# Optimization experiments

Measured on AMD Instinct MI355X. Metric: run time of the kernel, lower is better.

Reference implementation:

```python
import jax, jax.numpy as jnp
import numpy as np


def setup_inputs() -> dict:
    key = jax.random.key(0)
    ks = jax.random.split(key, 4)
    B, T, D, H = 64, 512, 512, 1024
    return {
        "x": jax.random.normal(ks[0], (B, T, D), dtype=jnp.float32),
        "kz": jax.random.normal(ks[1], (D, H), dtype=jnp.float32) * (1.0 / np.sqrt(D)),
        "kr": jax.random.normal(ks[2], (D, H), dtype=jnp.float32) * (1.0 / np.sqrt(D)),
        "kh": jax.random.normal(ks[3], (D, H), dtype=jnp.float32) * (1.0 / np.sqrt(D)),
        "mz": jnp.ones((H,), dtype=jnp.float32),
        "mr": jnp.ones((H,), dtype=jnp.float32),
        "br": jnp.zeros((H,), dtype=jnp.float32),
        "bz": jnp.zeros((H,), dtype=jnp.float32),
    }


def reference(x, kz, kr, kh, mz, mr, br, bz):
    B, T, D = x.shape
    H = kz.shape[1]
    # Precompute input projections for all timesteps (batched GEMMs),
    # identical math to per-step matmuls in the original cell.
    xz = jnp.einsum("btd,dh->bth", x, kz)  # [B,T,H]
    xr = jnp.einsum("btd,dh->bth", x, kr)
    xh = jnp.einsum("btd,dh->bth", x, kh)

    def step(h, inp):
        xz_t, xr_t, xh_t = inp  # each [B,H]
        r = jnp.tanh(xr_t + h * mr + br) + 1.0
        z = jax.nn.sigmoid(xz_t + h * mz + bz)
        h_new = z * h + (1.0 - z) * jnp.tanh(xh_t + r * h)
        return h_new, h_new

    h0 = jnp.zeros((B, H), dtype=x.dtype)
    # scan over time axis: move T to leading dim
    xs = (jnp.swapaxes(xz, 0, 1), jnp.swapaxes(xr, 0, 1), jnp.swapaxes(xh, 0, 1))
    _, ys = jax.lax.scan(step, h0, xs)  # ys: [T,B,H]
    return jnp.swapaxes(ys, 0, 1)  # [B,T,H]
```

## Files before the change

kernel.cpp:

```cpp
#include <hip/hip_runtime.h>
#include <hip/hip_bf16.h>
#include <math.h>


#define M_DIM 32768
#define K_DIM 512
#define H_DIM 1024
#define HPAD  1088
#define N3    3072

typedef _Float16 half8v __attribute__((ext_vector_type(8)));
typedef _Float16 half4v __attribute__((ext_vector_type(4)));
typedef float f32x4 __attribute__((ext_vector_type(4)));

__device__ __forceinline__ f32x4 mfma16(half8v a, half8v b, f32x4 c) {
    return __builtin_amdgcn_mfma_f32_16x16x32_f16(a, b, c, 0, 0, 0);
}

__device__ __forceinline__ void load_lds16(const void* g, void* l) {
    __builtin_amdgcn_global_load_lds(
        (const __attribute__((address_space(1))) void*)g,
        (__attribute__((address_space(3))) void*)l, 16, 0, 0);
}

__global__ __launch_bounds__(256) void convert_x(
    const float4* __restrict__ x4, half4v* __restrict__ hi4,
    half4v* __restrict__ lo4, int n4)
{
    int i = blockIdx.x * 256 + threadIdx.x;
    if (i >= n4) return;
    float4 v = x4[i];
    half4v h, lo;
    h.x = (_Float16)v.x; lo.x = (_Float16)(v.x - (float)h.x);
    h.y = (_Float16)v.y; lo.y = (_Float16)(v.y - (float)h.y);
    h.z = (_Float16)v.z; lo.z = (_Float16)(v.z - (float)h.z);
    h.w = (_Float16)v.w; lo.w = (_Float16)(v.w - (float)h.w);
    hi4[i] = h; lo4[i] = lo;
}

__global__ __launch_bounds__(256) void convert_wt_t(
    const float* __restrict__ kz, const float* __restrict__ kr,
    const float* __restrict__ kh, _Float16* __restrict__ wth,
    _Float16* __restrict__ wtl)
{
    __shared__ float lds[64][65];
    const int bid = blockIdx.x;
    const int w = bid >> 7;
    const int rem = bid & 127;
    const int k0 = (rem >> 4) * 64;
    const int n0 = (rem & 15) * 64;
    const int tid = threadIdx.x;
    const float* s = (w == 0) ? kz : ((w == 1) ? kr : kh);

#pragma unroll
    for (int r = 0; r < 4; ++r) {
        const int kk = (tid >> 4) + r * 16;
        const int nn = (tid & 15) * 4;
        float4 v = *(const float4*)&s[(size_t)(k0 + kk) * H_DIM + n0 + nn];
        lds[kk][nn + 0] = v.x; lds[kk][nn + 1] = v.y;
        lds[kk][nn + 2] = v.z; lds[kk][nn + 3] = v.w;
    }
    __syncthreads();
#pragma unroll
    for (int r = 0; r < 4; ++r) {
        const int nr = (tid >> 4) + r * 16;
        const int kb = (tid & 15) * 4;
        half4v hi, lo;
#pragma unroll
        for (int i = 0; i < 4; ++i) {
            float v = lds[kb + i][nr];
            _Float16 h = (_Float16)v;
            hi[i] = h; lo[i] = (_Float16)(v - (float)h);
        }
        const size_t o = ((size_t)(w * H_DIM + n0 + nr)) * K_DIM + k0 + kb;
        *(half4v*)&wth[o] = hi;
        *(half4v*)&wtl[o] = lo;
    }
}

template<bool PAD>
__global__ __launch_bounds__(256) void gemm_mfma_split(
    const _Float16* __restrict__ Ahi, const _Float16* __restrict__ Alo,
    const _Float16* __restrict__ Bthi, const _Float16* __restrict__ Btlo,
    float* __restrict__ XZ, float* __restrict__ XR, float* __restrict__ OUT)
{
    __shared__ _Float16 Ah[128 * 32];
    __shared__ _Float16 Al[128 * 32];
    __shared__ _Float16 Bh[128 * 32];
    __shared__ _Float16 Bl[128 * 32];

    const int tid = threadIdx.x;
    const int w = tid >> 6, l = tid & 63;
    const int l15 = l & 15, quad = l >> 4;
    const int bx = blockIdx.x, by = blockIdx.y;
    const long m0 = (long)by * 128;
    const long n0 = (long)bx * 128;

    f32x4 acc[4][4] = {};

    const int s1 = tid, s2 = tid + 256;
    const long aoff1 = (m0 + (s1 >> 2)) * K_DIM + (s1 & 3) * 8;
    const long aoff2 = (m0 + (s2 >> 2)) * K_DIM + (s2 & 3) * 8;
    const long boff1 = (n0 + (s1 >> 2)) * K_DIM + (s1 & 3) * 8;
    const long boff2 = (n0 + (s2 >> 2)) * K_DIM + (s2 & 3) * 8;

    const _Float16* a1 = Ahi + aoff1;  const _Float16* a2 = Ahi + aoff2;
    const _Float16* q1 = Alo + aoff1;  const _Float16* q2 = Alo + aoff2;
    const _Float16* b1 = Bthi + boff1; const _Float16* b2 = Bthi + boff2;
    const _Float16* c1 = Btlo + boff1; const _Float16* c2 = Btlo + boff2;

    _Float16* ldsA1 = &Ah[w * 512]; _Float16* ldsA2 = &Ah[2048 + w * 512];
    _Float16* ldsQ1 = &Al[w * 512]; _Float16* ldsQ2 = &Al[2048 + w * 512];
    _Float16* ldsB1 = &Bh[w * 512]; _Float16* ldsB2 = &Bh[2048 + w * 512];
    _Float16* ldsC1 = &Bl[w * 512]; _Float16* ldsC2 = &Bl[2048 + w * 512];

    const int wm = (w >> 1) * 64, wn = (w & 1) * 64;

    for (int kk = 0; kk < K_DIM / 32; ++kk) {
        load_lds16(a1, ldsA1); load_lds16(a2, ldsA2);
        load_lds16(q1, ldsQ1); load_lds16(q2, ldsQ2);
        load_lds16(b1, ldsB1); load_lds16(b2, ldsB2);
        load_lds16(c1, ldsC1); load_lds16(c2, ldsC2);
        a1 += 32; a2 += 32; q1 += 32; q2 += 32;
        b1 += 32; b2 += 32; c1 += 32; c2 += 32;
        __syncthreads();

        half8v afh[4], afl[4], bfh[4], bfl[4];
#pragma unroll
        for (int mi = 0; mi < 4; ++mi) {
            int row = (wm + mi * 16 + l15) * 32 + quad * 8;
            afh[mi] = *(const half8v*)&Ah[row];
            afl[mi] = *(const half8v*)&Al[row];
        }
#pragma unroll
        for (int ni = 0; ni < 4; ++ni) {
            int row = (wn + ni * 16 + l15) * 32 + quad * 8;
            bfh[ni] = *(const half8v*)&Bh[row];
            bfl[ni] = *(const half8v*)&Bl[row];
        }
#pragma unroll
        for (int mi = 0; mi < 4; ++mi)
#pragma unroll
            for (int ni = 0; ni < 4; ++ni) {
                acc[mi][ni] = mfma16(afh[mi], bfh[ni], acc[mi][ni]);
                acc[mi][ni] = mfma16(afh[mi], bfl[ni], acc[mi][ni]);
                acc[mi][ni] = mfma16(afl[mi], bfh[ni], acc[mi][ni]);
            }
        __syncthreads();
    }

    const long stride = PAD ? HPAD : H_DIM;
    float* dst = (bx < 8) ? XZ : ((bx < 16) ? XR : OUT);
    const long nl = (long)(bx & 7) * 128 + wn + l15;
#pragma unroll
    for (int mi = 0; mi < 4; ++mi) {
        const long m = m0 + wm + mi * 16 + quad * 4;
#pragma unroll
        for (int ni = 0; ni < 4; ++ni) {
            float* p = dst + m * stride + nl + ni * 16;
#pragma unroll
            for (int i = 0; i < 4; ++i)
                p[(long)i * stride] = acc[mi][ni][i];
        }
    }
}

#define BM 128
#define BN 128
#define BK 8
__global__ __launch_bounds__(256) void gemm_f32(
    const float* __restrict__ A, const float* __restrict__ B,
    float* __restrict__ C, int M, int N, int K)
{
    __shared__ float As[BK][BM];
    __shared__ float Bs[BK][BN];
    const int tid = threadIdx.x;
    const int bm = blockIdx.y * BM, bn = blockIdx.x * BN;
    const int tx = tid & 15, ty = tid >> 4;
    float acc[8][8];
#pragma unroll
    for (int i = 0; i < 8; i++)
#pragma unroll
        for (int j = 0; j < 8; j++) acc[i][j] = 0.f;
    const int a_row = tid >> 1, a_k = (tid & 1) * 4;
    const int b_row = tid >> 5, b_col = (tid & 31) * 4;
    const float* Aptr = A + (size_t)(bm + a_row) * K + a_k;
    const float* Bptr = B + (size_t)b_row * N + bn + b_col;
    for (int k0 = 0; k0 < K; k0 += BK) {
        float4 av = *(const float4*)(Aptr + k0);
        float4 bv = *(const float4*)(Bptr + (size_t)k0 * N);
        As[a_k + 0][a_row] = av.x; As[a_k + 1][a_row] = av.y;
        As[a_k + 2][a_row] = av.z; As[a_k + 3][a_row] = av.w;
        *(float4*)&Bs[b_row][b_col] = bv;
        __syncthreads();
#pragma unroll
        for (int kk = 0; kk < BK; kk++) {
            float4 a0 = *(const float4*)&As[kk][ty * 8];
            float4 a1 = *(const float4*)&As[kk][ty * 8 + 4];
            float4 b0 = *(const float4*)&Bs[kk][tx * 8];
            float4 b1 = *(const float4*)&Bs[kk][tx * 8 + 4];
            float a[8] = {a0.x, a0.y, a0.z, a0.w, a1.x, a1.y, a1.z, a1.w};
            float b[8] = {b0.x, b0.y, b0.z, b0.w, b1.x, b1.y, b1.z, b1.w};
#pragma unroll
            for (int i = 0; i < 8; i++)
#pragma unroll
                for (int j = 0; j < 8; j++)
                    acc[i][j] = fmaf(a[i], b[j], acc[i][j]);
        }
        __syncthreads();
    }
    float* Cptr = C + (size_t)(bm + ty * 8) * N + bn + tx * 8;
#pragma unroll
    for (int i = 0; i < 8; i++) {
        float4 c0 = {acc[i][0], acc[i][1], acc[i][2], acc[i][3]};
        float4 c1 = {acc[i][4], acc[i][5], acc[i][6], acc[i][7]};
        *(float4*)(Cptr + (size_t)i * N)     = c0;
        *(float4*)(Cptr + (size_t)i * N + 4) = c1;
    }
}

__device__ __forceinline__ float vrcp_nr(float d) {
    float r = __builtin_amdgcn_rcpf(d);
    return r * fmaf(-d, r, 2.0f);
}

__global__ __launch_bounds__(256) void scan_pad(
    const float* __restrict__ XZ, const float* __restrict__ XR,
    const float* __restrict__ XH, float* __restrict__ out,
    const float* __restrict__ mz, const float* __restrict__ mr,
    const float* __restrict__ br, const float* __restrict__ bz)
{
    const int gid = blockIdx.x * blockDim.x + threadIdx.x;
    const int b = gid >> 10;
    const int h = gid & (H_DIM - 1);

    const float mzK = -mz[h];
    const float mrK = -2.0f * mr[h];
    const float bzK = -bz[h];
    const float brK = -2.0f * br[h];
    float hs = 0.f;
    size_t ri = (size_t)b * 512 * HPAD + h;
    size_t wi = (size_t)b * 512 * H_DIM + h;

    float cz[16], cr[16], ch[16];
#pragma unroll
    for (int j = 0; j < 16; ++j) {
        cz[j] = bzK - XZ[ri + (size_t)j * HPAD];
        cr[j] = fmaf(-2.0f, XR[ri + (size_t)j * HPAD], brK);
        ch[j] = -2.0f * XH[ri + (size_t)j * HPAD];
    }
    for (int t0 = 0; t0 < 512; t0 += 16) {
        float nz[16], nr[16], nh[16];
        const bool more = (t0 + 16) < 512;
        const size_t nri = ri + 16ul * HPAD;
        if (more) {
#pragma unroll
            for (int j = 0; j < 16; ++j) {
                nz[j] = XZ[nri + (size_t)j * HPAD];
                nr[j] = XR[nri + (size_t)j * HPAD];
                nh[j] = XH[nri + (size_t)j * HPAD];
            }
        }
#pragma unroll
        for (int j = 0; j < 16; ++j) {
            const float u1   = fmaf(hs, mrK, cr[j]);
            const float uz   = fmaf(hs, mzK, cz[j]);
            const float hsK2 = -4.0f * hs;
            const float e1 = __expf(u1);
            const float s1 = vrcp_nr(e1 + 1.0f);
            const float ez = __expf(uz);
            const float sz = vrcp_nr(ez + 1.0f);
            const float u2 = fmaf(s1, hsK2, ch[j]);
            const float e2 = __expf(u2);
            const float s2 = vrcp_nr(e2 + 1.0f);
            const float th = fmaf(2.0f, s2, -1.0f);
            const float hn = fmaf(sz, hs - th, th);
            out[wi + (size_t)j * H_DIM] = hn;
            hs = hn;
        }
        ri = nri;
        wi += 16ul * H_DIM;
        if (more) {
#pragma unroll
            for (int j = 0; j < 16; ++j) {
                cz[j] = bzK - nz[j];
                cr[j] = fmaf(-2.0f, nr[j], brK);
                ch[j] = -2.0f * nh[j];
            }
        }
    }
}

__global__ __launch_bounds__(256) void scan_kernel(
    const float* __restrict__ XZ, const float* __restrict__ XR,
    float* __restrict__ OUT,
    const float* __restrict__ mz, const float* __restrict__ mr,
    const float* __restrict__ br, const float* __restrict__ bz)
{
    const int gid = blockIdx.x * blockDim.x + threadIdx.x;
    const int b = gid >> 10;
    const int h = gid & (H_DIM - 1);

    const float mzK = -mz[h];
    const float mrK = -2.0f * mr[h];
    const float bzK = -bz[h];
    const float brK = -2.0f * br[h];
    float hs = 0.f;
    size_t idx = (size_t)b * 512 * H_DIM + h;

    float cz[16], cr[16], ch[16];
#pragma unroll
    for (int j = 0; j < 16; ++j) {
        cz[j] = bzK - XZ[idx + (size_t)j * H_DIM];
        cr[j] = fmaf(-2.0f, XR[idx + (size_t)j * H_DIM], brK);
        ch[j] = -2.0f * OUT[idx + (size_t)j * H_DIM];
    }
    for (int t0 = 0; t0 < 512; t0 += 16) {
        float nz[16], nr[16], nh[16];
        const bool more = (t0 + 16) < 512;
        const size_t nidx = idx + 16ul * H_DIM;
        if (more) {
#pragma unroll
            for (int j = 0; j < 16; ++j) {
                nz[j] = XZ[nidx + (size_t)j * H_DIM];
                nr[j] = XR[nidx + (size_t)j * H_DIM];
                nh[j] = OUT[nidx + (size_t)j * H_DIM];
            }
        }
#pragma unroll
        for (int j = 0; j < 16; ++j) {
            const float u1   = fmaf(hs, mrK, cr[j]);
            const float uz   = fmaf(hs, mzK, cz[j]);
            const float hsK2 = -4.0f * hs;
            const float e1 = __expf(u1);
            const float s1 = vrcp_nr(e1 + 1.0f);
            const float ez = __expf(uz);
            const float sz = vrcp_nr(ez + 1.0f);
            const float u2 = fmaf(s1, hsK2, ch[j]);
            const float e2 = __expf(u2);
            const float s2 = vrcp_nr(e2 + 1.0f);
            const float th = fmaf(2.0f, s2, -1.0f);
            const float hn = fmaf(sz, hs - th, th);
            OUT[idx + (size_t)j * H_DIM] = hn;
            hs = hn;
        }
        idx = nidx;
        if (more) {
#pragma unroll
            for (int j = 0; j < 16; ++j) {
                cz[j] = bzK - nz[j];
                cr[j] = fmaf(-2.0f, nr[j], brK);
                ch[j] = -2.0f * nh[j];
            }
        }
    }
}

extern "C" void kernel_launch(void* const* d_in, const int* in_sizes, int n_in,
                              void* d_out, int out_size, void* d_ws, size_t ws_size,
                              hipStream_t stream) {
    const float* x  = (const float*)d_in[0];
    const float* kz = (const float*)d_in[1];
    const float* kr = (const float*)d_in[2];
    const float* kh = (const float*)d_in[3];
    const float* mz = (const float*)d_in[4];
    const float* mr = (const float*)d_in[5];
    const float* br = (const float*)d_in[6];
    const float* bz = (const float*)d_in[7];
    float* out = (float*)d_out;

    char* ws = (char*)d_ws;
    const int n4 = M_DIM * K_DIM / 4;

    const size_t PARR = (size_t)M_DIM * HPAD * 4ul;
    const size_t need_pad = 3ul * PARR + 67108864ul + 6291456ul;
    const size_t need_o   = 341835776ul;

    if (ws_size >= need_pad) {
        float* XZ = (float*)ws;
        float* XR = (float*)(ws + PARR);
        float* XH = (float*)(ws + 2 * PARR);
        _Float16* XHI = (_Float16*)(ws + 3 * PARR);
        _Float16* XLO = (_Float16*)(ws + 3 * PARR + 33554432ul);
        _Float16* WTH = (_Float16*)(ws + 3 * PARR + 67108864ul);
        _Float16* WTL = (_Float16*)(ws + 3 * PARR + 70254592ul);

        convert_x<<<n4 / 256, 256, 0, stream>>>(
            (const float4*)x, (half4v*)XHI, (half4v*)XLO, n4);
        convert_wt_t<<<384, 256, 0, stream>>>(kz, kr, kh, WTH, WTL);
        dim3 grid(N3 / 128, M_DIM / 128);
        gemm_mfma_split<true><<<grid, 256, 0, stream>>>(
            XHI, XLO, WTH, WTL, XZ, XR, XH);
        scan_pad<<<(64 * H_DIM) / 256, 256, 0, stream>>>(
            XZ, XR, XH, out, mz, mr, br, bz);
    } else if (ws_size >= need_o) {
        float* XZ = (float*)ws;
        float* XR = (float*)(ws + 134217728ul);
        _Float16* XHI = (_Float16*)(ws + 268435456ul);
        _Float16* XLO = (_Float16*)(ws + 301989888ul);
        _Float16* WTH = (_Float16*)(ws + 335544320ul);
        _Float16* WTL = (_Float16*)(ws + 338690048ul);

        convert_x<<<n4 / 256, 256, 0, stream>>>(
            (const float4*)x, (half4v*)XHI, (half4v*)XLO, n4);
        convert_wt_t<<<384, 256, 0, stream>>>(kz, kr, kh, WTH, WTL);
        dim3 grid(N3 / 128, M_DIM / 128);
        gemm_mfma_split<false><<<grid, 256, 0, stream>>>(
            XHI, XLO, WTH, WTL, XZ, XR, out);
        scan_kernel<<<(64 * H_DIM) / 256, 256, 0, stream>>>(
            XZ, XR, out, mz, mr, br, bz);
    } else {
        float* XZ = (float*)ws;
        float* XR = (float*)(ws + 134217728ul);
        dim3 grid(H_DIM / BN, M_DIM / BM);
        gemm_f32<<<grid, 256, 0, stream>>>(x, kz, XZ,  M_DIM, H_DIM, K_DIM);
        gemm_f32<<<grid, 256, 0, stream>>>(x, kr, XR,  M_DIM, H_DIM, K_DIM);
        gemm_f32<<<grid, 256, 0, stream>>>(x, kh, out, M_DIM, H_DIM, K_DIM);
        scan_kernel<<<(64 * H_DIM) / 256, 256, 0, stream>>>(
            XZ, XR, out, mz, mr, br, bz);
    }
}
```

Baseline: 587.3 us.

## Interleave gate projections into grouped per-block layout for scan locality

The GEMM epilogue now writes the three gate projections into a single interleaved buffer laid out as [batch][256-wide h-group][t][gate*256+h]. The scan reads each timestep's z, r and h inputs from one contiguous 3 KB row per block instead of three separate padded arrays. This replaces the HPAD padding trick for avoiding channel/bank conflicts with locality, so each block streams a compact region. The trade-off is more scattered GEMM stores, and it relies on the workspace being large enough.

```diff
diff --git a/kernel.cpp b/kernel.cpp
--- a/kernel.cpp
+++ b/kernel.cpp
@@ -6,8 +6,8 @@
 #define M_DIM 32768
 #define K_DIM 512
 #define H_DIM 1024
-#define HPAD  1088
 #define N3    3072
+#define GS    768
 
 typedef _Float16 half8v __attribute__((ext_vector_type(8)));
 typedef _Float16 half4v __attribute__((ext_vector_type(4)));
@@ -78,7 +78,7 @@
     }
 }
 
-template<bool PAD>
+template<int LAYOUT>
 __global__ __launch_bounds__(256) void gemm_mfma_split(
     const _Float16* __restrict__ Ahi, const _Float16* __restrict__ Alo,
     const _Float16* __restrict__ Bthi, const _Float16* __restrict__ Btlo,
@@ -149,18 +149,38 @@
         __syncthreads();
     }
 
-    const long stride = PAD ? HPAD : H_DIM;
-    float* dst = (bx < 8) ? XZ : ((bx < 16) ? XR : OUT);
-    const long nl = (long)(bx & 7) * 128 + wn + l15;
-#pragma unroll
-    for (int mi = 0; mi < 4; ++mi) {
-        const long m = m0 + wm + mi * 16 + quad * 4;
-#pragma unroll
-        for (int ni = 0; ni < 4; ++ni) {
-            float* p = dst + m * stride + nl + ni * 16;
-#pragma unroll
-            for (int i = 0; i < 4; ++i)
-                p[(long)i * stride] = acc[mi][ni][i];
+    if (LAYOUT == 0) {
+        float* dst = (bx < 8) ? XZ : ((bx < 16) ? XR : OUT);
+        const long nl = (long)(bx & 7) * 128 + wn + l15;
+#pragma unroll
+        for (int mi = 0; mi < 4; ++mi) {
+            const long m = m0 + wm + mi * 16 + quad * 4;
+#pragma unroll
+            for (int ni = 0; ni < 4; ++ni) {
+                float* p = dst + m * H_DIM + nl + ni * 16;
+#pragma unroll
+                for (int i = 0; i < 4; ++i)
+                    p[(long)i * H_DIM] = acc[mi][ni][i];
+            }
+        }
+    } else {
+        float* XI = XZ;
+        const int gate = bx >> 3;
+        const long n   = (long)(bx & 7) * 128 + wn + l15;
+        const long hh  = n >> 8;
+        const long nlo = n & 255;
+#pragma unroll
+        for (int mi = 0; mi < 4; ++mi) {
+            const long m = m0 + wm + mi * 16 + quad * 4;
+            const long b = m >> 9;
+            const long t = m & 511;
+            float* p = XI + ((b * 4 + hh) * 512 + t) * GS + gate * 256 + nlo;
+#pragma unroll
+            for (int ni = 0; ni < 4; ++ni) {
+#pragma unroll
+                for (int i = 0; i < 4; ++i)
+                    p[(long)i * GS + ni * 16] = acc[mi][ni][i];
+            }
         }
     }
 }
@@ -224,43 +244,45 @@
     return r * fmaf(-d, r, 2.0f);
 }
 
-__global__ __launch_bounds__(256) void scan_pad(
-    const float* __restrict__ XZ, const float* __restrict__ XR,
-    const float* __restrict__ XH, float* __restrict__ out,
+__global__ __launch_bounds__(256) void scan_gs(
+    const float* __restrict__ XI, float* __restrict__ out,
     const float* __restrict__ mz, const float* __restrict__ mr,
     const float* __restrict__ br, const float* __restrict__ bz)
 {
-    const int gid = blockIdx.x * blockDim.x + threadIdx.x;
-    const int b = gid >> 10;
-    const int h = gid & (H_DIM - 1);
+    const int bid = blockIdx.x;
+    const int b = bid >> 2, hh = bid & 3;
+    const int tid = threadIdx.x;
+    const int h = hh * 256 + tid;
 
     const float mzK = -mz[h];
     const float mrK = -2.0f * mr[h];
     const float bzK = -bz[h];
     const float brK = -2.0f * br[h];
     float hs = 0.f;
-    size_t ri = (size_t)b * 512 * HPAD + h;
-    size_t wi = (size_t)b * 512 * H_DIM + h;
+
+    const float* base = XI + ((size_t)(b * 4 + hh) * 512) * GS + tid;
+    float* const po = out + ((size_t)b << 19) + h;
 
     float cz[16], cr[16], ch[16];
 #pragma unroll
     for (int j = 0; j < 16; ++j) {
-        cz[j] = bzK - XZ[ri + (size_t)j * HPAD];
-        cr[j] = fmaf(-2.0f, XR[ri + (size_t)j * HPAD], brK);
-        ch[j] = -2.0f * XH[ri + (size_t)j * HPAD];
+        const float* p = base + (size_t)j * GS;
+        cz[j] = bzK - p[0];
+        cr[j] = fmaf(-2.0f, p[256], brK);
+        ch[j] = -2.0f * p[512];
     }
     for (int t0 = 0; t0 < 512; t0 += 16) {
         float nz[16], nr[16], nh[16];
         const bool more = (t0 + 16) < 512;
-        const size_t nri = ri + 16ul * HPAD;
         if (more) {
+            const float* pb = base + (size_t)(t0 + 16) * GS;
 #pragma unroll
             for (int j = 0; j < 16; ++j) {
-                nz[j] = XZ[nri + (size_t)j * HPAD];
-                nr[j] = XR[nri + (size_t)j * HPAD];
-                nh[j] = XH[nri + (size_t)j * HPAD];
-            }
-        }
+                const float* p = pb + (size_t)j * GS;
+                nz[j] = p[0]; nr[j] = p[256]; nh[j] = p[512];
+            }
+        }
+        float* pout = po + ((size_t)t0 << 10);
 #pragma unroll
         for (int j = 0; j < 16; ++j) {
             const float u1   = fmaf(hs, mrK, cr[j]);
@@ -275,11 +297,9 @@
             const float s2 = vrcp_nr(e2 + 1.0f);
             const float th = fmaf(2.0f, s2, -1.0f);
             const float hn = fmaf(sz, hs - th, th);
-            out[wi + (size_t)j * H_DIM] = hn;
+            *pout = hn; pout += H_DIM;
             hs = hn;
         }
-        ri = nri;
-        wi += 16ul * H_DIM;
         if (more) {
 #pragma unroll
             for (int j = 0; j < 16; ++j) {
@@ -372,27 +392,24 @@
     char* ws = (char*)d_ws;
     const int n4 = M_DIM * K_DIM / 4;
 
-    const size_t PARR = (size_t)M_DIM * HPAD * 4ul;
-    const size_t need_pad = 3ul * PARR + 67108864ul + 6291456ul;
-    const size_t need_o   = 341835776ul;
-
-    if (ws_size >= need_pad) {
-        float* XZ = (float*)ws;
-        float* XR = (float*)(ws + PARR);
-        float* XH = (float*)(ws + 2 * PARR);
-        _Float16* XHI = (_Float16*)(ws + 3 * PARR);
-        _Float16* XLO = (_Float16*)(ws + 3 * PARR + 33554432ul);
-        _Float16* WTH = (_Float16*)(ws + 3 * PARR + 67108864ul);
-        _Float16* WTL = (_Float16*)(ws + 3 * PARR + 70254592ul);
+    const size_t XI_BYTES = (size_t)M_DIM * N3 * 4ul;
+    const size_t need_gs = XI_BYTES + 67108864ul + 6291456ul;
+    const size_t need_o  = 341835776ul;
+
+    if (ws_size >= need_gs) {
+        float* XI = (float*)ws;
+        _Float16* XHI = (_Float16*)(ws + XI_BYTES);
+        _Float16* XLO = (_Float16*)(ws + XI_BYTES + 33554432ul);
+        _Float16* WTH = (_Float16*)(ws + XI_BYTES + 67108864ul);
+        _Float16* WTL = (_Float16*)(ws + XI_BYTES + 70254592ul);
 
         convert_x<<<n4 / 256, 256, 0, stream>>>(
             (const float4*)x, (half4v*)XHI, (half4v*)XLO, n4);
         convert_wt_t<<<384, 256, 0, stream>>>(kz, kr, kh, WTH, WTL);
         dim3 grid(N3 / 128, M_DIM / 128);
-        gemm_mfma_split<true><<<grid, 256, 0, stream>>>(
-            XHI, XLO, WTH, WTL, XZ, XR, XH);
-        scan_pad<<<(64 * H_DIM) / 256, 256, 0, stream>>>(
-            XZ, XR, XH, out, mz, mr, br, bz);
+        gemm_mfma_split<1><<<grid, 256, 0, stream>>>(
+            XHI, XLO, WTH, WTL, XI, nullptr, nullptr);
+        scan_gs<<<256, 256, 0, stream>>>(XI, out, mz, mr, br, bz);
     } else if (ws_size >= need_o) {
         float* XZ = (float*)ws;
         float* XR = (float*)(ws + 134217728ul);
@@ -405,7 +422,7 @@
             (const float4*)x, (half4v*)XHI, (half4v*)XLO, n4);
         convert_wt_t<<<384, 256, 0, stream>>>(kz, kr, kh, WTH, WTL);
         dim3 grid(N3 / 128, M_DIM / 128);
-        gemm_mfma_split<false><<<grid, 256, 0, stream>>>(
+        gemm_mfma_split<0><<<grid, 256, 0, stream>>>(
             XHI, XLO, WTH, WTL, XZ, XR, out);
         scan_kernel<<<(64 * H_DIM) / 256, 256, 0, stream>>>(
             XZ, XR, out, mz, mr, br, bz);
```

Result: no change. 595.6 us (+1.4%).
